# Performance work log

Hardware: AMD Instinct MI355X
Metric: run time of the kernel (lower is better)

Reference implementation:

```python
import jax, jax.numpy as jnp
from jax import lax
import numpy as np

T, B, X, Y = 24, 16, 32, 32
FS, FM, FC = 64, 16, 16
I = FS + FM + FC  # GRU input size = 96
H = 32            # hidden_size


def setup_inputs() -> dict:
    key = jax.random.key(0)
    ks = jax.random.split(key, 8)
    s = 1.0 / np.sqrt(H)  # pytorch GRU init scale
    return {
        "spatial": jax.random.normal(ks[0], (B, X, Y, FS), jnp.float32),
        "meteorology": jax.random.normal(ks[1], (T, B, X, Y, FM), jnp.float32),
        "context": jax.random.normal(ks[2], (T, B, X, Y, FC), jnp.float32),
        "W_ih": jax.random.uniform(ks[3], (3 * H, I), jnp.float32, -s, s),
        "W_hh": jax.random.uniform(ks[4], (3 * H, H), jnp.float32, -s, s),
        "b_ih": jax.random.uniform(ks[5], (3 * H,), jnp.float32, -s, s),
        "b_hh": jax.random.uniform(ks[6], (3 * H,), jnp.float32, -s, s),
        "W": jax.random.normal(ks[7], (H, FS), jnp.float32),
    }


def _gru_final_state(x, W_ih, W_hh, b_ih, b_hh):
    # x: (T, N, I); returns final hidden state (N, H). PyTorch GRU cell math.
    n_batch = x.shape[1]
    h0 = jnp.zeros((n_batch, H), x.dtype)

    def step(h, xt):
        gi = xt @ W_ih.T + b_ih          # (N, 3H)
        gh = h @ W_hh.T + b_hh           # (N, 3H)
        i_r, i_z, i_n = jnp.split(gi, 3, axis=-1)
        h_r, h_z, h_n = jnp.split(gh, 3, axis=-1)
        r = jax.nn.sigmoid(i_r + h_r)
        z = jax.nn.sigmoid(i_z + h_z)
        n = jnp.tanh(i_n + r * h_n)
        h_new = (1.0 - z) * n + z * h
        return h_new, None

    hT, _ = lax.scan(step, h0, x)
    return hT


def reference(spatial, meteorology, context, W_ih, W_hh, b_ih, b_hh, W):
    # Broadcast static spatial features over time and concat along feature dim.
    t = meteorology.shape[0]
    sp = jnp.broadcast_to(spatial[None], (t,) + spatial.shape)
    x = jnp.concatenate([sp, meteorology, context], axis=-1)  # (T,B,X,Y,I)
    # Batch all spatial positions into one recurrence: (T, B*X*Y, I)
    x = x.reshape(t, B * X * Y, I)
    hT = _gru_final_state(x, W_ih, W_hh, b_ih, b_hh)          # (B*X*Y, H)
    out = hT @ W                                              # (B*X*Y, FS)
    return out.reshape(B, X, Y, FS)
```

## Files before the change

### kernel.cpp

```cpp
#include <hip/hip_runtime.h>
#include <hip/hip_fp16.h>
#include <math.h>


typedef __attribute__((ext_vector_type(8))) short short8;
typedef __attribute__((ext_vector_type(8))) _Float16 half8;
typedef __attribute__((ext_vector_type(4))) float f32x4;

#define NSEQ 16384
#define TSTEPS 24
#define LOG2E 1.44269504088896340736f

#define P_HH   0
#define P_MC   3072
#define P_SP   6144
#define P_WP_H 12288
#define P_WP_L 14336
#define P_BIAS 16384

__device__ __forceinline__ int sigma_inv(int ks) {
  int cc = ks >> 3, e = ks & 7;
  return (e < 4) ? (4 * cc + e) : (16 + 4 * cc + (e - 4));
}

__global__ void pack_w(const float* __restrict__ W_ih,
                       const float* __restrict__ W_hh,
                       const float* __restrict__ b_ih,
                       const float* __restrict__ b_hh,
                       const float* __restrict__ Wp,
                       unsigned short* __restrict__ ws) {
  int idx = blockIdx.x * blockDim.x + threadIdx.x;
  for (int i = idx; i < 14464; i += gridDim.x * blockDim.x) {
    if (i < 3072) {
      int row = i >> 5, ks = i & 31;
      float sc = (row < 64) ? LOG2E : (2.0f * LOG2E);
      float v = W_hh[row * 32 + sigma_inv(ks)] * sc;
      ws[P_HH + i] = __half_as_ushort(__float2half(v));
    } else if (i < 6144) {
      int j = i - 3072;
      int row = j >> 5, k = j & 31;
      float sc = (row < 64) ? LOG2E : (2.0f * LOG2E);
      ws[P_MC + j] = __half_as_ushort(__float2half(W_ih[row * 96 + 64 + k] * sc));
    } else if (i < 12288) {
      int j = i - 6144;
      int row = j >> 6, k = j & 63;
      float sc = (row < 64) ? LOG2E : (2.0f * LOG2E);
      ws[P_SP + j] = __half_as_ushort(__float2half(W_ih[row * 96 + k] * sc));
    } else if (i < 14336) {
      int j = i - 12288;
      int frow = j >> 5, ks = j & 31;
      float v = Wp[sigma_inv(ks) * 64 + frow];
      __half h = __float2half(v);
      float lo = v - __half2float(h);
      ws[P_WP_H + j] = __half_as_ushort(h);
      ws[P_WP_L + j] = __half_as_ushort(__float2half(lo));
    } else {
      int k = i - 14336;
      float* bb = (float*)(ws + P_BIAS);
      if (k < 96) {
        float sc = (k < 64) ? LOG2E : (2.0f * LOG2E);
        bb[k] = (b_ih[k] + (k < 64 ? b_hh[k] : 0.0f)) * sc;
      } else {
        bb[k] = 2.0f * LOG2E * b_hh[64 + (k - 96)];
      }
    }
  }
}

__device__ __forceinline__ float exp2_fast(float x) {
#if __has_builtin(__builtin_amdgcn_exp2f)
  return __builtin_amdgcn_exp2f(x);
#else
  return __expf(x * 0.6931471805599453f);
#endif
}

__device__ __forceinline__ unsigned int pk_f16(float a, float b) {
#if __has_builtin(__builtin_amdgcn_cvt_pkrtz)
  auto r = __builtin_amdgcn_cvt_pkrtz(a, b);
  return __builtin_bit_cast(unsigned int, r);
#else
  return (unsigned)__half_as_ushort(__float2half(a)) |
         ((unsigned)__half_as_ushort(__float2half(b)) << 16);
#endif
}

__device__ __forceinline__ f32x4 mfma_h(half8 a, half8 b, f32x4 c) {
  return __builtin_amdgcn_mfma_f32_16x16x32_f16(a, b, c, 0, 0, 0);
}

__device__ __forceinline__ void barrier_lds() {
  asm volatile("s_waitcnt lgkmcnt(0)" ::: "memory");
  __builtin_amdgcn_s_barrier();
}

union S8u { short8 v; unsigned int u[4]; };
union H8u { half8 v; unsigned int u[4]; };

__global__ __launch_bounds__(128, 2)
void gru4(const float* __restrict__ spatial,
          const float* __restrict__ met,
          const float* __restrict__ ctx,
          const unsigned short* __restrict__ ws,
          float* __restrict__ out) {
  __shared__ unsigned int hbuf[2][2][64][2];

  const int tid = threadIdx.x;
  const int lane = tid & 63;
  const int p = tid >> 6;
  const int l15 = lane & 15;
  const int c = lane >> 4;
  const int seq = blockIdx.x * 16 + l15;

  ((unsigned int*)hbuf[1])[tid] = 0u;
  ((unsigned int*)hbuf[1])[tid + 128] = 0u;

  half8 whh[3], wmc[3];
#pragma unroll
  for (int g = 0; g < 3; ++g) {
    int off = (g * 32 + p * 16 + l15) * 32 + c * 8;
    S8u t0; t0.v = *(const short8*)(ws + P_HH + off);
    H8u h0; h0.u[0]=t0.u[0]; h0.u[1]=t0.u[1]; h0.u[2]=t0.u[2]; h0.u[3]=t0.u[3];
    whh[g] = h0.v;
    S8u t1; t1.v = *(const short8*)(ws + P_MC + off);
    H8u h1; h1.u[0]=t1.u[0]; h1.u[1]=t1.u[1]; h1.u[2]=t1.u[2]; h1.u[3]=t1.u[3];
    wmc[g] = h1.v;
  }

  const float* bb = (const float*)(ws + P_BIAS);
  f32x4 acc_i[3], bhn4;
#pragma unroll
  for (int g = 0; g < 3; ++g) {
    float4 v = *(const float4*)(bb + g * 32 + p * 16 + 4 * c);
    acc_i[g][0] = v.x; acc_i[g][1] = v.y; acc_i[g][2] = v.z; acc_i[g][3] = v.w;
  }
  {
    float4 v = *(const float4*)(bb + 96 + p * 16 + 4 * c);
    bhn4[0] = v.x; bhn4[1] = v.y; bhn4[2] = v.z; bhn4[3] = v.w;
  }

#pragma unroll
  for (int kt = 0; kt < 2; ++kt) {
    const float* sp = spatial + (size_t)seq * 64 + kt * 32 + c * 8;
    float4 a0 = *(const float4*)sp;
    float4 a1 = *(const float4*)(sp + 4);
    H8u sf;
    sf.u[0] = pk_f16(a0.x, a0.y); sf.u[1] = pk_f16(a0.z, a0.w);
    sf.u[2] = pk_f16(a1.x, a1.y); sf.u[3] = pk_f16(a1.z, a1.w);
#pragma unroll
    for (int g = 0; g < 3; ++g) {
      int row = g * 32 + p * 16 + l15;
      S8u t; t.v = *(const short8*)(ws + P_SP + row * 64 + kt * 32 + c * 8);
      H8u wv; wv.u[0]=t.u[0]; wv.u[1]=t.u[1]; wv.u[2]=t.u[2]; wv.u[3]=t.u[3];
      acc_i[g] = mfma_h(wv.v, sf.v, acc_i[g]);
    }
  }

  const float* lptr = ((c < 2) ? met : ctx) + (size_t)seq * 16 + (c & 1) * 8;

  f32x4 xacc[3];
  {
    float4 a0 = *(const float4*)lptr;
    float4 a1 = *(const float4*)(lptr + 4);
    H8u xf;
    xf.u[0] = pk_f16(a0.x, a0.y); xf.u[1] = pk_f16(a0.z, a0.w);
    xf.u[2] = pk_f16(a1.x, a1.y); xf.u[3] = pk_f16(a1.z, a1.w);
#pragma unroll
    for (int g = 0; g < 3; ++g) xacc[g] = mfma_h(wmc[g], xf.v, acc_i[g]);
  }
  float4 xs0a = *(const float4*)(lptr + (size_t)1 * NSEQ * 16);
  float4 xs0b = *(const float4*)(lptr + (size_t)1 * NSEQ * 16 + 4);
  float4 xs1a = *(const float4*)(lptr + (size_t)2 * NSEQ * 16);
  float4 xs1b = *(const float4*)(lptr + (size_t)2 * NSEQ * 16 + 4);

  float hst[4] = {0.f, 0.f, 0.f, 0.f};
  unsigned int own0 = 0u, own1 = 0u;
  const f32x4 zero4 = {0.f, 0.f, 0.f, 0.f};

  barrier_lds();

#pragma unroll 2
  for (int t = 0; t < TSTEPS; ++t) {
    const unsigned int* hp = &hbuf[(t + 1) & 1][1 - p][lane][0];
    unsigned int phx = hp[0], phy = hp[1];

    H8u fh;
    fh.u[0] = p ? phx : own0;  fh.u[1] = p ? phy : own1;
    fh.u[2] = p ? own0 : phx;  fh.u[3] = p ? own1 : phy;

    f32x4 d0 = mfma_h(whh[0], fh.v, xacc[0]);
    f32x4 d1 = mfma_h(whh[1], fh.v, xacc[1]);
    f32x4 dn = mfma_h(whh[2], fh.v, bhn4);
    f32x4 ti = xacc[2];

    {
      float4 xa = (t & 1) ? xs1a : xs0a;
      float4 xb = (t & 1) ? xs1b : xs0b;
      H8u xf;
      xf.u[0] = pk_f16(xa.x, xa.y); xf.u[1] = pk_f16(xa.z, xa.w);
      xf.u[2] = pk_f16(xb.x, xb.y); xf.u[3] = pk_f16(xb.z, xb.w);
#pragma unroll
      for (int g = 0; g < 3; ++g) xacc[g] = mfma_h(wmc[g], xf.v, acc_i[g]);
      int tf = (t + 3 < TSTEPS) ? (t + 3) : (TSTEPS - 1);
      float4 na = *(const float4*)(lptr + (size_t)tf * NSEQ * 16);
      float4 nb = *(const float4*)(lptr + (size_t)tf * NSEQ * 16 + 4);
      if (t & 1) { xs1a = na; xs1b = nb; } else { xs0a = na; xs0b = nb; }
    }

    float hv_[4];
#pragma unroll
    for (int q = 0; q < 4; ++q) {
      float r = __builtin_amdgcn_rcpf(1.0f + exp2_fast(-d0[q]));
      float z = __builtin_amdgcn_rcpf(1.0f + exp2_fast(-d1[q]));
      float Y = fmaf(r, dn[q], ti[q]);
      float e = exp2_fast(-Y);
      float nn = fmaf(2.0f, __builtin_amdgcn_rcpf(1.0f + e), -1.0f);
      float hv = fmaf(z, hst[q] - nn, nn);
      hst[q] = hv;
      hv_[q] = hv;
    }
    own0 = pk_f16(hv_[0], hv_[1]);
    own1 = pk_f16(hv_[2], hv_[3]);
    hbuf[t & 1][p][lane][0] = own0;
    hbuf[t & 1][p][lane][1] = own1;

    barrier_lds();
  }

  H8u fh;
  {
    const unsigned int* hp = &hbuf[1][1 - p][lane][0];
    unsigned int phx = hp[0], phy = hp[1];
    fh.u[0] = p ? phx : own0;  fh.u[1] = p ? phy : own1;
    fh.u[2] = p ? own0 : phx;  fh.u[3] = p ? own1 : phy;
  }

#pragma unroll
  for (int pt = 0; pt < 2; ++pt) {
    int ftile = pt * 2 + p;
    int off = (ftile * 16 + l15) * 32 + c * 8;
    S8u t0; t0.v = *(const short8*)(ws + P_WP_H + off);
    H8u wph; wph.u[0]=t0.u[0]; wph.u[1]=t0.u[1]; wph.u[2]=t0.u[2]; wph.u[3]=t0.u[3];
    S8u t1; t1.v = *(const short8*)(ws + P_WP_L + off);
    H8u wpl; wpl.u[0]=t1.u[0]; wpl.u[1]=t1.u[1]; wpl.u[2]=t1.u[2]; wpl.u[3]=t1.u[3];
    f32x4 o = mfma_h(wph.v, fh.v, zero4);
    o = mfma_h(wpl.v, fh.v, o);
    float* op = out + (size_t)seq * 64 + ftile * 16 + 4 * c;
    *(float4*)op = make_float4(o[0], o[1], o[2], o[3]);
  }
}

extern "C" void kernel_launch(void* const* d_in, const int* in_sizes, int n_in,
                              void* d_out, int out_size, void* d_ws, size_t ws_size,
                              hipStream_t stream) {
  const float* spatial = (const float*)d_in[0];
  const float* met     = (const float*)d_in[1];
  const float* ctx     = (const float*)d_in[2];
  const float* W_ih    = (const float*)d_in[3];
  const float* W_hh    = (const float*)d_in[4];
  const float* b_ih    = (const float*)d_in[5];
  const float* b_hh    = (const float*)d_in[6];
  const float* Wp      = (const float*)d_in[7];
  float* out = (float*)d_out;
  unsigned short* ws = (unsigned short*)d_ws;

  hipLaunchKernelGGL(pack_w, dim3(57), dim3(256), 0, stream,
                     W_ih, W_hh, b_ih, b_hh, Wp, ws);
  hipLaunchKernelGGL(gru4, dim3(1024), dim3(128), 0, stream,
                     spatial, met, ctx, ws, out);
}
```

Measured before the change: 26.73 us.

## Split GRU block into producer waves for input projection and consumer recurrence waves

Doubles the block to four waves. Two producer waves compute the input projections (spatial plus meteorology/context) for each timestep and stage them in a double-buffered LDS array. Two consumer waves read those values and run only the hidden-state recurrence and the output projection. The aim is to take the input MFMAs and global loads off the serial recurrence critical path. The cost is extra LDS traffic, a larger block, and barriers that every wave must hit in lockstep.

```diff
diff --git a/kernel.cpp b/kernel.cpp
--- a/kernel.cpp
+++ b/kernel.cpp
@@ -97,156 +97,172 @@
 union S8u { short8 v; unsigned int u[4]; };
 union H8u { half8 v; unsigned int u[4]; };
 
-__global__ __launch_bounds__(128, 2)
-void gru4(const float* __restrict__ spatial,
+__global__ __launch_bounds__(256, 4)
+void gru5(const float* __restrict__ spatial,
           const float* __restrict__ met,
           const float* __restrict__ ctx,
           const unsigned short* __restrict__ ws,
           float* __restrict__ out) {
+  __shared__ float xls[2][6][16][20];
   __shared__ unsigned int hbuf[2][2][64][2];
 
   const int tid = threadIdx.x;
   const int lane = tid & 63;
-  const int p = tid >> 6;
+  const int wv = tid >> 6;
   const int l15 = lane & 15;
   const int c = lane >> 4;
   const int seq = blockIdx.x * 16 + l15;
+  const float* bb = (const float*)(ws + P_BIAS);
+  const f32x4 zero4 = {0.f, 0.f, 0.f, 0.f};
 
   ((unsigned int*)hbuf[1])[tid] = 0u;
-  ((unsigned int*)hbuf[1])[tid + 128] = 0u;
-
-  half8 whh[3], wmc[3];
-#pragma unroll
-  for (int g = 0; g < 3; ++g) {
-    int off = (g * 32 + p * 16 + l15) * 32 + c * 8;
-    S8u t0; t0.v = *(const short8*)(ws + P_HH + off);
-    H8u h0; h0.u[0]=t0.u[0]; h0.u[1]=t0.u[1]; h0.u[2]=t0.u[2]; h0.u[3]=t0.u[3];
-    whh[g] = h0.v;
-    S8u t1; t1.v = *(const short8*)(ws + P_MC + off);
-    H8u h1; h1.u[0]=t1.u[0]; h1.u[1]=t1.u[1]; h1.u[2]=t1.u[2]; h1.u[3]=t1.u[3];
-    wmc[g] = h1.v;
-  }
-
-  const float* bb = (const float*)(ws + P_BIAS);
-  f32x4 acc_i[3], bhn4;
-#pragma unroll
-  for (int g = 0; g < 3; ++g) {
-    float4 v = *(const float4*)(bb + g * 32 + p * 16 + 4 * c);
-    acc_i[g][0] = v.x; acc_i[g][1] = v.y; acc_i[g][2] = v.z; acc_i[g][3] = v.w;
-  }
-  {
-    float4 v = *(const float4*)(bb + 96 + p * 16 + 4 * c);
-    bhn4[0] = v.x; bhn4[1] = v.y; bhn4[2] = v.z; bhn4[3] = v.w;
-  }
-
-#pragma unroll
-  for (int kt = 0; kt < 2; ++kt) {
-    const float* sp = spatial + (size_t)seq * 64 + kt * 32 + c * 8;
-    float4 a0 = *(const float4*)sp;
-    float4 a1 = *(const float4*)(sp + 4);
-    H8u sf;
-    sf.u[0] = pk_f16(a0.x, a0.y); sf.u[1] = pk_f16(a0.z, a0.w);
-    sf.u[2] = pk_f16(a1.x, a1.y); sf.u[3] = pk_f16(a1.z, a1.w);
+
+  if (wv >= 2) {
+    const int q = wv - 2;
+    half8 wmc[3];
+    f32x4 acc_i[3];
 #pragma unroll
     for (int g = 0; g < 3; ++g) {
-      int row = g * 32 + p * 16 + l15;
-      S8u t; t.v = *(const short8*)(ws + P_SP + row * 64 + kt * 32 + c * 8);
-      H8u wv; wv.u[0]=t.u[0]; wv.u[1]=t.u[1]; wv.u[2]=t.u[2]; wv.u[3]=t.u[3];
-      acc_i[g] = mfma_h(wv.v, sf.v, acc_i[g]);
-    }
-  }
-
-  const float* lptr = ((c < 2) ? met : ctx) + (size_t)seq * 16 + (c & 1) * 8;
-
-  f32x4 xacc[3];
-  {
-    float4 a0 = *(const float4*)lptr;
-    float4 a1 = *(const float4*)(lptr + 4);
-    H8u xf;
-    xf.u[0] = pk_f16(a0.x, a0.y); xf.u[1] = pk_f16(a0.z, a0.w);
-    xf.u[2] = pk_f16(a1.x, a1.y); xf.u[3] = pk_f16(a1.z, a1.w);
-#pragma unroll
-    for (int g = 0; g < 3; ++g) xacc[g] = mfma_h(wmc[g], xf.v, acc_i[g]);
-  }
-  float4 xs0a = *(const float4*)(lptr + (size_t)1 * NSEQ * 16);
-  float4 xs0b = *(const float4*)(lptr + (size_t)1 * NSEQ * 16 + 4);
-  float4 xs1a = *(const float4*)(lptr + (size_t)2 * NSEQ * 16);
-  float4 xs1b = *(const float4*)(lptr + (size_t)2 * NSEQ * 16 + 4);
-
-  float hst[4] = {0.f, 0.f, 0.f, 0.f};
-  unsigned int own0 = 0u, own1 = 0u;
-  const f32x4 zero4 = {0.f, 0.f, 0.f, 0.f};
-
-  barrier_lds();
+      int off = (g * 32 + q * 16 + l15) * 32 + c * 8;
+      S8u t1; t1.v = *(const short8*)(ws + P_MC + off);
+      H8u h1; h1.u[0]=t1.u[0]; h1.u[1]=t1.u[1]; h1.u[2]=t1.u[2]; h1.u[3]=t1.u[3];
+      wmc[g] = h1.v;
+      float4 v = *(const float4*)(bb + g * 32 + q * 16 + 4 * c);
+      acc_i[g][0] = v.x; acc_i[g][1] = v.y; acc_i[g][2] = v.z; acc_i[g][3] = v.w;
+    }
+#pragma unroll
+    for (int kt = 0; kt < 2; ++kt) {
+      const float* sp = spatial + (size_t)seq * 64 + kt * 32 + c * 8;
+      float4 a0 = *(const float4*)sp;
+      float4 a1 = *(const float4*)(sp + 4);
+      H8u sf;
+      sf.u[0] = pk_f16(a0.x, a0.y); sf.u[1] = pk_f16(a0.z, a0.w);
+      sf.u[2] = pk_f16(a1.x, a1.y); sf.u[3] = pk_f16(a1.z, a1.w);
+#pragma unroll
+      for (int g = 0; g < 3; ++g) {
+        int row = g * 32 + q * 16 + l15;
+        S8u t; t.v = *(const short8*)(ws + P_SP + row * 64 + kt * 32 + c * 8);
+        H8u w2; w2.u[0]=t.u[0]; w2.u[1]=t.u[1]; w2.u[2]=t.u[2]; w2.u[3]=t.u[3];
+        acc_i[g] = mfma_h(w2.v, sf.v, acc_i[g]);
+      }
+    }
+    const float* lptr = ((c < 2) ? met : ctx) + (size_t)seq * 16 + (c & 1) * 8;
+    {
+      float4 a0 = *(const float4*)lptr;
+      float4 a1 = *(const float4*)(lptr + 4);
+      H8u xf;
+      xf.u[0] = pk_f16(a0.x, a0.y); xf.u[1] = pk_f16(a0.z, a0.w);
+      xf.u[2] = pk_f16(a1.x, a1.y); xf.u[3] = pk_f16(a1.z, a1.w);
+#pragma unroll
+      for (int g = 0; g < 3; ++g) {
+        f32x4 D = mfma_h(wmc[g], xf.v, acc_i[g]);
+        *(f32x4*)&xls[0][g * 2 + q][l15][c * 4] = D;
+      }
+    }
+    float4 xs0a = *(const float4*)(lptr + (size_t)1 * NSEQ * 16);
+    float4 xs0b = *(const float4*)(lptr + (size_t)1 * NSEQ * 16 + 4);
+    float4 xs1a = *(const float4*)(lptr + (size_t)2 * NSEQ * 16);
+    float4 xs1b = *(const float4*)(lptr + (size_t)2 * NSEQ * 16 + 4);
+
+    barrier_lds();
 
 #pragma unroll 2
-  for (int t = 0; t < TSTEPS; ++t) {
-    const unsigned int* hp = &hbuf[(t + 1) & 1][1 - p][lane][0];
-    unsigned int phx = hp[0], phy = hp[1];
-
-    H8u fh;
-    fh.u[0] = p ? phx : own0;  fh.u[1] = p ? phy : own1;
-    fh.u[2] = p ? own0 : phx;  fh.u[3] = p ? own1 : phy;
-
-    f32x4 d0 = mfma_h(whh[0], fh.v, xacc[0]);
-    f32x4 d1 = mfma_h(whh[1], fh.v, xacc[1]);
-    f32x4 dn = mfma_h(whh[2], fh.v, bhn4);
-    f32x4 ti = xacc[2];
-
-    {
+    for (int t = 0; t < TSTEPS; ++t) {
       float4 xa = (t & 1) ? xs1a : xs0a;
       float4 xb = (t & 1) ? xs1b : xs0b;
       H8u xf;
       xf.u[0] = pk_f16(xa.x, xa.y); xf.u[1] = pk_f16(xa.z, xa.w);
       xf.u[2] = pk_f16(xb.x, xb.y); xf.u[3] = pk_f16(xb.z, xb.w);
-#pragma unroll
-      for (int g = 0; g < 3; ++g) xacc[g] = mfma_h(wmc[g], xf.v, acc_i[g]);
-      int tf = (t + 3 < TSTEPS) ? (t + 3) : (TSTEPS - 1);
-      float4 na = *(const float4*)(lptr + (size_t)tf * NSEQ * 16);
-      float4 nb = *(const float4*)(lptr + (size_t)tf * NSEQ * 16 + 4);
-      if (t & 1) { xs1a = na; xs1b = nb; } else { xs0a = na; xs0b = nb; }
-    }
-
-    float hv_[4];
-#pragma unroll
-    for (int q = 0; q < 4; ++q) {
-      float r = __builtin_amdgcn_rcpf(1.0f + exp2_fast(-d0[q]));
-      float z = __builtin_amdgcn_rcpf(1.0f + exp2_fast(-d1[q]));
-      float Y = fmaf(r, dn[q], ti[q]);
-      float e = exp2_fast(-Y);
-      float nn = fmaf(2.0f, __builtin_amdgcn_rcpf(1.0f + e), -1.0f);
-      float hv = fmaf(z, hst[q] - nn, nn);
-      hst[q] = hv;
-      hv_[q] = hv;
-    }
-    own0 = pk_f16(hv_[0], hv_[1]);
-    own1 = pk_f16(hv_[2], hv_[3]);
-    hbuf[t & 1][p][lane][0] = own0;
-    hbuf[t & 1][p][lane][1] = own1;
+      {
+        int tf = (t + 3 < TSTEPS) ? (t + 3) : (TSTEPS - 1);
+        float4 na = *(const float4*)(lptr + (size_t)tf * NSEQ * 16);
+        float4 nb = *(const float4*)(lptr + (size_t)tf * NSEQ * 16 + 4);
+        if (t & 1) { xs1a = na; xs1b = nb; } else { xs0a = na; xs0b = nb; }
+      }
+      const int buf = (t + 1) & 1;
+#pragma unroll
+      for (int g = 0; g < 3; ++g) {
+        f32x4 D = mfma_h(wmc[g], xf.v, acc_i[g]);
+        *(f32x4*)&xls[buf][g * 2 + q][l15][c * 4] = D;
+      }
+      barrier_lds();
+    }
+  } else {
+    const int p = wv;
+    half8 whh[3];
+#pragma unroll
+    for (int g = 0; g < 3; ++g) {
+      int off = (g * 32 + p * 16 + l15) * 32 + c * 8;
+      S8u t0; t0.v = *(const short8*)(ws + P_HH + off);
+      H8u h0; h0.u[0]=t0.u[0]; h0.u[1]=t0.u[1]; h0.u[2]=t0.u[2]; h0.u[3]=t0.u[3];
+      whh[g] = h0.v;
+    }
+    f32x4 bhn4;
+    {
+      float4 v = *(const float4*)(bb + 96 + p * 16 + 4 * c);
+      bhn4[0] = v.x; bhn4[1] = v.y; bhn4[2] = v.z; bhn4[3] = v.w;
+    }
+    float hst[4] = {0.f, 0.f, 0.f, 0.f};
+    unsigned int own0 = 0u, own1 = 0u;
 
     barrier_lds();
-  }
-
-  H8u fh;
-  {
-    const unsigned int* hp = &hbuf[1][1 - p][lane][0];
-    unsigned int phx = hp[0], phy = hp[1];
-    fh.u[0] = p ? phx : own0;  fh.u[1] = p ? phy : own1;
-    fh.u[2] = p ? own0 : phx;  fh.u[3] = p ? own1 : phy;
-  }
-
-#pragma unroll
-  for (int pt = 0; pt < 2; ++pt) {
-    int ftile = pt * 2 + p;
-    int off = (ftile * 16 + l15) * 32 + c * 8;
-    S8u t0; t0.v = *(const short8*)(ws + P_WP_H + off);
-    H8u wph; wph.u[0]=t0.u[0]; wph.u[1]=t0.u[1]; wph.u[2]=t0.u[2]; wph.u[3]=t0.u[3];
-    S8u t1; t1.v = *(const short8*)(ws + P_WP_L + off);
-    H8u wpl; wpl.u[0]=t1.u[0]; wpl.u[1]=t1.u[1]; wpl.u[2]=t1.u[2]; wpl.u[3]=t1.u[3];
-    f32x4 o = mfma_h(wph.v, fh.v, zero4);
-    o = mfma_h(wpl.v, fh.v, o);
-    float* op = out + (size_t)seq * 64 + ftile * 16 + 4 * c;
-    *(float4*)op = make_float4(o[0], o[1], o[2], o[3]);
+
+#pragma unroll 2
+    for (int t = 0; t < TSTEPS; ++t) {
+      const unsigned int* hp = &hbuf[(t + 1) & 1][1 - p][lane][0];
+      unsigned int phx = hp[0], phy = hp[1];
+      f32x4 xr = *(const f32x4*)&xls[t & 1][p][l15][c * 4];
+      f32x4 xz = *(const f32x4*)&xls[t & 1][2 + p][l15][c * 4];
+      f32x4 ti = *(const f32x4*)&xls[t & 1][4 + p][l15][c * 4];
+
+      H8u fh;
+      fh.u[0] = p ? phx : own0;  fh.u[1] = p ? phy : own1;
+      fh.u[2] = p ? own0 : phx;  fh.u[3] = p ? own1 : phy;
+
+      f32x4 d0 = mfma_h(whh[0], fh.v, xr);
+      f32x4 d1 = mfma_h(whh[1], fh.v, xz);
+      f32x4 dn = mfma_h(whh[2], fh.v, bhn4);
+
+      float hv_[4];
+#pragma unroll
+      for (int qq = 0; qq < 4; ++qq) {
+        float r = __builtin_amdgcn_rcpf(1.0f + exp2_fast(-d0[qq]));
+        float z = __builtin_amdgcn_rcpf(1.0f + exp2_fast(-d1[qq]));
+        float Y = fmaf(r, dn[qq], ti[qq]);
+        float e = exp2_fast(-Y);
+        float nn = fmaf(2.0f, __builtin_amdgcn_rcpf(1.0f + e), -1.0f);
+        float hv = fmaf(z, hst[qq] - nn, nn);
+        hst[qq] = hv;
+        hv_[qq] = hv;
+      }
+      own0 = pk_f16(hv_[0], hv_[1]);
+      own1 = pk_f16(hv_[2], hv_[3]);
+      hbuf[t & 1][p][lane][0] = own0;
+      hbuf[t & 1][p][lane][1] = own1;
+
+      barrier_lds();
+    }
+
+    H8u fh;
+    {
+      const unsigned int* hp = &hbuf[1][1 - p][lane][0];
+      unsigned int phx = hp[0], phy = hp[1];
+      fh.u[0] = p ? phx : own0;  fh.u[1] = p ? phy : own1;
+      fh.u[2] = p ? own0 : phx;  fh.u[3] = p ? own1 : phy;
+    }
+#pragma unroll
+    for (int pt = 0; pt < 2; ++pt) {
+      int ftile = pt * 2 + p;
+      int off = (ftile * 16 + l15) * 32 + c * 8;
+      S8u t0; t0.v = *(const short8*)(ws + P_WP_H + off);
+      H8u wph; wph.u[0]=t0.u[0]; wph.u[1]=t0.u[1]; wph.u[2]=t0.u[2]; wph.u[3]=t0.u[3];
+      S8u t1; t1.v = *(const short8*)(ws + P_WP_L + off);
+      H8u wpl; wpl.u[0]=t1.u[0]; wpl.u[1]=t1.u[1]; wpl.u[2]=t1.u[2]; wpl.u[3]=t1.u[3];
+      f32x4 o = mfma_h(wph.v, fh.v, zero4);
+      o = mfma_h(wpl.v, fh.v, o);
+      float* op = out + (size_t)seq * 64 + ftile * 16 + 4 * c;
+      *(float4*)op = make_float4(o[0], o[1], o[2], o[3]);
+    }
   }
 }
 
@@ -266,6 +282,6 @@
 
   hipLaunchKernelGGL(pack_w, dim3(57), dim3(256), 0, stream,
                      W_ih, W_hh, b_ih, b_hh, Wp, ws);
-  hipLaunchKernelGGL(gru4, dim3(1024), dim3(128), 0, stream,
+  hipLaunchKernelGGL(gru5, dim3(1024), dim3(256), 0, stream,
                      spatial, met, ctx, ws, out);
 }
```

After: 26.27 us. No clear change (-1.7%).

## Give each wave the full hidden state and drop the LDS exchange

Applied to the files above, without the earlier changes.

Each wave now computes all 32 hidden units for its 16 sequences, using 6 MFMA tiles per gate set instead of 3. Before, two waves split the hidden dimension and swapped halves of h through LDS with a barrier every timestep. The new layout keeps h entirely in registers and removes the per-step LDS round trip and block barrier. In exchange, the grid has half as many waves, each doing twice the work and holding more registers, which lowers the latency-hiding parallelism per SIMD.

```diff
diff --git a/kernel.cpp b/kernel.cpp
--- a/kernel.cpp
+++ b/kernel.cpp
@@ -89,54 +89,47 @@
   return __builtin_amdgcn_mfma_f32_16x16x32_f16(a, b, c, 0, 0, 0);
 }
 
-__device__ __forceinline__ void barrier_lds() {
-  asm volatile("s_waitcnt lgkmcnt(0)" ::: "memory");
-  __builtin_amdgcn_s_barrier();
-}
-
 union S8u { short8 v; unsigned int u[4]; };
 union H8u { half8 v; unsigned int u[4]; };
 
-__global__ __launch_bounds__(128, 2)
-void gru4(const float* __restrict__ spatial,
+__global__ __launch_bounds__(256)
+void gru6(const float* __restrict__ spatial,
           const float* __restrict__ met,
           const float* __restrict__ ctx,
           const unsigned short* __restrict__ ws,
           float* __restrict__ out) {
-  __shared__ unsigned int hbuf[2][2][64][2];
-
   const int tid = threadIdx.x;
   const int lane = tid & 63;
-  const int p = tid >> 6;
+  const int wv = tid >> 6;
   const int l15 = lane & 15;
   const int c = lane >> 4;
-  const int seq = blockIdx.x * 16 + l15;
-
-  ((unsigned int*)hbuf[1])[tid] = 0u;
-  ((unsigned int*)hbuf[1])[tid + 128] = 0u;
-
-  half8 whh[3], wmc[3];
-#pragma unroll
-  for (int g = 0; g < 3; ++g) {
-    int off = (g * 32 + p * 16 + l15) * 32 + c * 8;
+  const int seq = blockIdx.x * 64 + wv * 16 + l15;
+  const float* bb = (const float*)(ws + P_BIAS);
+  const f32x4 zero4 = {0.f, 0.f, 0.f, 0.f};
+
+  half8 whh[6], wmc[6];
+#pragma unroll
+  for (int j = 0; j < 6; ++j) {
+    int off = (j * 16 + l15) * 32 + c * 8;
     S8u t0; t0.v = *(const short8*)(ws + P_HH + off);
     H8u h0; h0.u[0]=t0.u[0]; h0.u[1]=t0.u[1]; h0.u[2]=t0.u[2]; h0.u[3]=t0.u[3];
-    whh[g] = h0.v;
+    whh[j] = h0.v;
     S8u t1; t1.v = *(const short8*)(ws + P_MC + off);
     H8u h1; h1.u[0]=t1.u[0]; h1.u[1]=t1.u[1]; h1.u[2]=t1.u[2]; h1.u[3]=t1.u[3];
-    wmc[g] = h1.v;
-  }
-
-  const float* bb = (const float*)(ws + P_BIAS);
-  f32x4 acc_i[3], bhn4;
-#pragma unroll
-  for (int g = 0; g < 3; ++g) {
-    float4 v = *(const float4*)(bb + g * 32 + p * 16 + 4 * c);
-    acc_i[g][0] = v.x; acc_i[g][1] = v.y; acc_i[g][2] = v.z; acc_i[g][3] = v.w;
+    wmc[j] = h1.v;
+  }
+
+  f32x4 acc_i[6], bhnA, bhnB;
+#pragma unroll
+  for (int j = 0; j < 6; ++j) {
+    float4 v = *(const float4*)(bb + j * 16 + 4 * c);
+    acc_i[j][0] = v.x; acc_i[j][1] = v.y; acc_i[j][2] = v.z; acc_i[j][3] = v.w;
   }
   {
-    float4 v = *(const float4*)(bb + 96 + p * 16 + 4 * c);
-    bhn4[0] = v.x; bhn4[1] = v.y; bhn4[2] = v.z; bhn4[3] = v.w;
+    float4 va = *(const float4*)(bb + 96 + 4 * c);
+    float4 vb = *(const float4*)(bb + 96 + 16 + 4 * c);
+    bhnA[0] = va.x; bhnA[1] = va.y; bhnA[2] = va.z; bhnA[3] = va.w;
+    bhnB[0] = vb.x; bhnB[1] = vb.y; bhnB[2] = vb.z; bhnB[3] = vb.w;
   }
 
 #pragma unroll
@@ -148,17 +141,17 @@
     sf.u[0] = pk_f16(a0.x, a0.y); sf.u[1] = pk_f16(a0.z, a0.w);
     sf.u[2] = pk_f16(a1.x, a1.y); sf.u[3] = pk_f16(a1.z, a1.w);
 #pragma unroll
-    for (int g = 0; g < 3; ++g) {
-      int row = g * 32 + p * 16 + l15;
+    for (int j = 0; j < 6; ++j) {
+      int row = j * 16 + l15;
       S8u t; t.v = *(const short8*)(ws + P_SP + row * 64 + kt * 32 + c * 8);
-      H8u wv; wv.u[0]=t.u[0]; wv.u[1]=t.u[1]; wv.u[2]=t.u[2]; wv.u[3]=t.u[3];
-      acc_i[g] = mfma_h(wv.v, sf.v, acc_i[g]);
+      H8u w2; w2.u[0]=t.u[0]; w2.u[1]=t.u[1]; w2.u[2]=t.u[2]; w2.u[3]=t.u[3];
+      acc_i[j] = mfma_h(w2.v, sf.v, acc_i[j]);
     }
   }
 
   const float* lptr = ((c < 2) ? met : ctx) + (size_t)seq * 16 + (c & 1) * 8;
 
-  f32x4 xacc[3];
+  f32x4 xacc[6];
   {
     float4 a0 = *(const float4*)lptr;
     float4 a1 = *(const float4*)(lptr + 4);
@@ -166,32 +159,30 @@
     xf.u[0] = pk_f16(a0.x, a0.y); xf.u[1] = pk_f16(a0.z, a0.w);
     xf.u[2] = pk_f16(a1.x, a1.y); xf.u[3] = pk_f16(a1.z, a1.w);
 #pragma unroll
-    for (int g = 0; g < 3; ++g) xacc[g] = mfma_h(wmc[g], xf.v, acc_i[g]);
+    for (int j = 0; j < 6; ++j) xacc[j] = mfma_h(wmc[j], xf.v, acc_i[j]);
   }
   float4 xs0a = *(const float4*)(lptr + (size_t)1 * NSEQ * 16);
   float4 xs0b = *(const float4*)(lptr + (size_t)1 * NSEQ * 16 + 4);
   float4 xs1a = *(const float4*)(lptr + (size_t)2 * NSEQ * 16);
   float4 xs1b = *(const float4*)(lptr + (size_t)2 * NSEQ * 16 + 4);
 
-  float hst[4] = {0.f, 0.f, 0.f, 0.f};
-  unsigned int own0 = 0u, own1 = 0u;
-  const f32x4 zero4 = {0.f, 0.f, 0.f, 0.f};
-
-  barrier_lds();
+  float hst[8];
+#pragma unroll
+  for (int i = 0; i < 8; ++i) hst[i] = 0.0f;
+  H8u fh;
+#pragma unroll
+  for (int i = 0; i < 4; ++i) fh.u[i] = 0u;
 
 #pragma unroll 2
   for (int t = 0; t < TSTEPS; ++t) {
-    const unsigned int* hp = &hbuf[(t + 1) & 1][1 - p][lane][0];
-    unsigned int phx = hp[0], phy = hp[1];
-
-    H8u fh;
-    fh.u[0] = p ? phx : own0;  fh.u[1] = p ? phy : own1;
-    fh.u[2] = p ? own0 : phx;  fh.u[3] = p ? own1 : phy;
-
-    f32x4 d0 = mfma_h(whh[0], fh.v, xacc[0]);
-    f32x4 d1 = mfma_h(whh[1], fh.v, xacc[1]);
-    f32x4 dn = mfma_h(whh[2], fh.v, bhn4);
-    f32x4 ti = xacc[2];
+    f32x4 ti0 = xacc[4], ti1 = xacc[5];
+
+    f32x4 dr0 = mfma_h(whh[0], fh.v, xacc[0]);
+    f32x4 dr1 = mfma_h(whh[1], fh.v, xacc[1]);
+    f32x4 dz0 = mfma_h(whh[2], fh.v, xacc[2]);
+    f32x4 dz1 = mfma_h(whh[3], fh.v, xacc[3]);
+    f32x4 th0 = mfma_h(whh[4], fh.v, bhnA);
+    f32x4 th1 = mfma_h(whh[5], fh.v, bhnB);
 
     {
       float4 xa = (t & 1) ? xs1a : xs0a;
@@ -200,52 +191,49 @@
       xf.u[0] = pk_f16(xa.x, xa.y); xf.u[1] = pk_f16(xa.z, xa.w);
       xf.u[2] = pk_f16(xb.x, xb.y); xf.u[3] = pk_f16(xb.z, xb.w);
 #pragma unroll
-      for (int g = 0; g < 3; ++g) xacc[g] = mfma_h(wmc[g], xf.v, acc_i[g]);
+      for (int j = 0; j < 6; ++j) xacc[j] = mfma_h(wmc[j], xf.v, acc_i[j]);
       int tf = (t + 3 < TSTEPS) ? (t + 3) : (TSTEPS - 1);
       float4 na = *(const float4*)(lptr + (size_t)tf * NSEQ * 16);
       float4 nb = *(const float4*)(lptr + (size_t)tf * NSEQ * 16 + 4);
       if (t & 1) { xs1a = na; xs1b = nb; } else { xs0a = na; xs0b = nb; }
     }
 
-    float hv_[4];
-#pragma unroll
-    for (int q = 0; q < 4; ++q) {
-      float r = __builtin_amdgcn_rcpf(1.0f + exp2_fast(-d0[q]));
-      float z = __builtin_amdgcn_rcpf(1.0f + exp2_fast(-d1[q]));
-      float Y = fmaf(r, dn[q], ti[q]);
-      float e = exp2_fast(-Y);
-      float nn = fmaf(2.0f, __builtin_amdgcn_rcpf(1.0f + e), -1.0f);
-      float hv = fmaf(z, hst[q] - nn, nn);
-      hst[q] = hv;
-      hv_[q] = hv;
-    }
-    own0 = pk_f16(hv_[0], hv_[1]);
-    own1 = pk_f16(hv_[2], hv_[3]);
-    hbuf[t & 1][p][lane][0] = own0;
-    hbuf[t & 1][p][lane][1] = own1;
-
-    barrier_lds();
-  }
-
-  H8u fh;
-  {
-    const unsigned int* hp = &hbuf[1][1 - p][lane][0];
-    unsigned int phx = hp[0], phy = hp[1];
-    fh.u[0] = p ? phx : own0;  fh.u[1] = p ? phy : own1;
-    fh.u[2] = p ? own0 : phx;  fh.u[3] = p ? own1 : phy;
-  }
-
-#pragma unroll
-  for (int pt = 0; pt < 2; ++pt) {
-    int ftile = pt * 2 + p;
-    int off = (ftile * 16 + l15) * 32 + c * 8;
+    float hv_[8];
+#pragma unroll
+    for (int jj = 0; jj < 2; ++jj) {
+      f32x4 ddr = jj ? dr1 : dr0;
+      f32x4 ddz = jj ? dz1 : dz0;
+      f32x4 tth = jj ? th1 : th0;
+      f32x4 tti = jj ? ti1 : ti0;
+#pragma unroll
+      for (int q = 0; q < 4; ++q) {
+        int i = jj * 4 + q;
+        float r = __builtin_amdgcn_rcpf(1.0f + exp2_fast(-ddr[q]));
+        float z = __builtin_amdgcn_rcpf(1.0f + exp2_fast(-ddz[q]));
+        float Y = fmaf(r, tth[q], tti[q]);
+        float e = exp2_fast(-Y);
+        float nn = fmaf(2.0f, __builtin_amdgcn_rcpf(1.0f + e), -1.0f);
+        float hv = fmaf(z, hst[i] - nn, nn);
+        hst[i] = hv;
+        hv_[i] = hv;
+      }
+    }
+    fh.u[0] = pk_f16(hv_[0], hv_[1]);
+    fh.u[1] = pk_f16(hv_[2], hv_[3]);
+    fh.u[2] = pk_f16(hv_[4], hv_[5]);
+    fh.u[3] = pk_f16(hv_[6], hv_[7]);
+  }
+
+#pragma unroll
+  for (int pt = 0; pt < 4; ++pt) {
+    int off = (pt * 16 + l15) * 32 + c * 8;
     S8u t0; t0.v = *(const short8*)(ws + P_WP_H + off);
     H8u wph; wph.u[0]=t0.u[0]; wph.u[1]=t0.u[1]; wph.u[2]=t0.u[2]; wph.u[3]=t0.u[3];
     S8u t1; t1.v = *(const short8*)(ws + P_WP_L + off);
     H8u wpl; wpl.u[0]=t1.u[0]; wpl.u[1]=t1.u[1]; wpl.u[2]=t1.u[2]; wpl.u[3]=t1.u[3];
     f32x4 o = mfma_h(wph.v, fh.v, zero4);
     o = mfma_h(wpl.v, fh.v, o);
-    float* op = out + (size_t)seq * 64 + ftile * 16 + 4 * c;
+    float* op = out + (size_t)seq * 64 + pt * 16 + 4 * c;
     *(float4*)op = make_float4(o[0], o[1], o[2], o[3]);
   }
 }
@@ -266,6 +254,6 @@
 
   hipLaunchKernelGGL(pack_w, dim3(57), dim3(256), 0, stream,
                      W_ih, W_hh, b_ih, b_hh, Wp, ws);
-  hipLaunchKernelGGL(gru4, dim3(1024), dim3(128), 0, stream,
+  hipLaunchKernelGGL(gru6, dim3(256), dim3(256), 0, stream,
                      spatial, met, ctx, ws, out);
 }
```

Result: slower. 31.50 us (+17.8%).
